# Kernel optimization log

Measured on AMD Instinct MI355X. Metric: run time of the kernel, lower is better.

## Reference

```python
import jax, jax.numpy as jnp
import numpy as np
from jax import lax

MASK_STEEP = 4.0
MASK_SHIFT = 0.5
RESIST_TH = 0.225
RESIST_STEEP = 50.0
MAX_DOSE = 1.02
MIN_DOSE = 0.98
KD = 35  # kernel_dim1 == kernel_dim2


def setup_inputs() -> dict:
    key = jax.random.key(0)
    ks = jax.random.split(key, 7)
    N, H, W, K = 2, 1024, 1024, 24
    return {
        "mask_tile": jax.random.uniform(ks[0], (N, 1, H, W), dtype=jnp.float32),
        "kernel_focus_r": jax.random.normal(ks[1], (K, KD, KD), dtype=jnp.float32) * 0.02,
        "kernel_focus_i": jax.random.normal(ks[2], (K, KD, KD), dtype=jnp.float32) * 0.02,
        "kernel_defocus_r": jax.random.normal(ks[3], (K, KD, KD), dtype=jnp.float32) * 0.02,
        "kernel_defocus_i": jax.random.normal(ks[4], (K, KD, KD), dtype=jnp.float32) * 0.02,
        "kernel_focus_scale": jax.random.uniform(ks[5], (K, 1, 1), dtype=jnp.float32),
        "kernel_defocus_scale": jax.random.uniform(ks[6], (K, 1, 1), dtype=jnp.float32),
    }


def _avepool3(x):
    # nn.AvgPool2d(kernel=3, stride=1, pad=1) with count_include_pad=True ==
    # conv with a 3x3 ones/9 kernel and zero padding.
    k = jnp.ones((1, 1, 3, 3), x.dtype) / 9.0
    return lax.conv_general_dilated(
        x, k, window_strides=(1, 1), padding=[(1, 1), (1, 1)],
        dimension_numbers=("NCHW", "OIHW", "NCHW"))


def _dose_branch(spec, dose, kernel, scale, h, w):
    # spec: [N,1,KD,KD] complex; kernel: [K,KD,KD] complex; scale: [K,1,1]
    x = (spec * dose) * kernel[None]                 # [N,K,KD,KD] (repeat_interleave via broadcast, C=1)
    x = jnp.fft.ifft2(x, s=(h, w))                   # zero-pad to full tile, [N,K,h,w] complex
    inten = (x.real * x.real + x.imag * x.imag) * scale[None]
    inten = jnp.sum(inten, axis=1, keepdims=True)    # [N,1,h,w]
    resist = jax.nn.sigmoid(RESIST_STEEP * (inten - RESIST_TH))
    return resist, inten


def reference(mask_tile, kernel_focus_r, kernel_focus_i, kernel_defocus_r,
              kernel_defocus_i, kernel_focus_scale, kernel_defocus_scale):
    n, _, h, w = mask_tile.shape
    off = h // 2 - KD // 2
    mask = _avepool3(mask_tile)
    mask = jax.nn.sigmoid(MASK_STEEP * (mask - MASK_SHIFT))
    mf = jnp.fft.fftshift(jnp.fft.fft2(mask), axes=(-2, -1))  # [N,1,h,w] complex64
    spec = mf[:, :, off:off + KD, off:off + KD]               # [N,1,KD,KD]
    kf = kernel_focus_r + 1j * kernel_focus_i
    kdf = kernel_defocus_r + 1j * kernel_defocus_i
    nominal, x_out = _dose_branch(spec, 1.0, kf, kernel_focus_scale, h, w)
    outer, x_out_max = _dose_branch(spec, MAX_DOSE, kf, kernel_focus_scale, h, w)
    inner, x_out_min = _dose_branch(spec, MIN_DOSE, kdf, kernel_defocus_scale, h, w)
    return (nominal, inner, outer, x_out, x_out_min, x_out_max)
```

## Files before the change

kernel.cpp:

```cpp
#include <hip/hip_runtime.h>
#include <math.h>

#define NBATCH 2
#define HH 1024
#define WW 1024
#define KKER 24
#define KDIM 35
#define NPIX (HH*WW)
#define KSQ (KDIM*KDIM)
#define NDA 69
#define NCH 7

#define TW_OFF   0
#define G_OFF    2048
#define SPEC_OFF (G_OFF + NBATCH*HH*KDIM*2)
#define VP_OFF   (SPEC_OFF + NBATCH*KSQ*2)
#define V_OFF    (VP_OFF + NBATCH*2*KKER*NCH*NDA*KDIM*2)
#define U_OFF    (V_OFF + NBATCH*2*NDA*KDIM*2)

__device__ __forceinline__ float2 cmadd(float2 p, float2 w, float2 u) {
    return make_float2(fmaf(p.x, w.x, fmaf(-p.y, w.y, u.x)),
                       fmaf(p.x, w.y, fmaf( p.y, w.x, u.y)));
}
__device__ __forceinline__ float sigm(float v) {
    return 1.f / (1.f + expf(-v));
}

__global__ void build_tw(float* __restrict__ ws) {
    int j = blockIdx.x * blockDim.x + threadIdx.x;
    if (j < 1024) {
        float s, c;
        sincospif(-2.0f * (float)j / 1024.0f, &s, &c);
        ws[TW_OFF + 2*j]     = c;
        ws[TW_OFF + 2*j + 1] = s;
    }
}

__global__ __launch_bounds__(512) void fwd_rows(const float* __restrict__ mt, float* __restrict__ ws) {
    __shared__ __align__(16) float vs[1024];
    __shared__ float row[1024];
    __shared__ float twl[2048];
    __shared__ float P[560 * 2];
    int bid = blockIdx.x;
    int n = bid >> 10, y = bid & 1023;
    int t = threadIdx.x;
    const float* base = mt + (size_t)n * NPIX;
    const float4* r0 = (y > 0)    ? (const float4*)(base + (size_t)(y - 1) * WW) : nullptr;
    const float4* r1 =              (const float4*)(base + (size_t)y * WW);
    const float4* r2 = (y < 1023) ? (const float4*)(base + (size_t)(y + 1) * WW) : nullptr;
    if (t < 256) {
        float4 a = r1[t];
        if (r0) { float4 b = r0[t]; a.x += b.x; a.y += b.y; a.z += b.z; a.w += b.w; }
        if (r2) { float4 b = r2[t]; a.x += b.x; a.y += b.y; a.z += b.z; a.w += b.w; }
        ((float4*)vs)[t] = a;
    }
    for (int i = t; i < 2048; i += 512) twl[i] = ws[TW_OFF + i];
    __syncthreads();
    for (int x = t; x < 1024; x += 512) {
        float s = vs[x];
        if (x > 0)    s += vs[x - 1];
        if (x < 1023) s += vs[x + 1];
        s *= (1.0f / 9.0f);
        row[x] = sigm(4.0f * (s - 0.5f));
    }
    __syncthreads();
    for (int task = t; task < 560; task += 512) {
        int q = task / KDIM, v = task - q * KDIM;
        int m = v - 17;
        unsigned jm = ((unsigned)m) & 1023u;
        float cmr = twl[2*jm], cmi = twl[2*jm + 1];
        float ar = 0.f, ai = 0.f;
        #pragma unroll
        for (int sc = 0; sc < 2; ++sc) {
            int xs = q * 64 + sc * 32;
            unsigned j0 = ((unsigned)(m * xs)) & 1023u;
            float wr = twl[2*j0], wi = twl[2*j0 + 1];
            #pragma unroll
            for (int i = 0; i < 32; ++i) {
                float val = row[xs + i];
                ar = fmaf(val, wr, ar);
                ai = fmaf(val, wi, ai);
                float nwr = fmaf(wr, cmr, -wi * cmi);
                float nwi = fmaf(wr, cmi,  wi * cmr);
                wr = nwr; wi = nwi;
            }
        }
        P[task * 2]     = ar;
        P[task * 2 + 1] = ai;
    }
    __syncthreads();
    if (t < KDIM) {
        float gr = 0.f, gi = 0.f;
        #pragma unroll
        for (int q = 0; q < 16; ++q) {
            gr += P[(q * KDIM + t) * 2];
            gi += P[(q * KDIM + t) * 2 + 1];
        }
        float* Gp = ws + G_OFF + ((size_t)(n * HH + y) * KDIM + t) * 2;
        Gp[0] = gr; Gp[1] = gi;
    }
}

__global__ __launch_bounds__(320) void fwd_cols(float* __restrict__ ws) {
    __shared__ float twl[2048];
    __shared__ float P[280 * 2];
    int bid = blockIdx.x;
    int n = bid / KDIM, a = bid - n * KDIM;
    int t = threadIdx.x;
    for (int i = t; i < 2048; i += 320) twl[i] = ws[TW_OFF + i];
    __syncthreads();
    int q = t / 40, b = t - 40 * q;
    if (b < KDIM) {
        int ma = a - 17;
        int y0 = q * 128;
        float ar = 0.f, ai = 0.f;
        for (int i = 0; i < 128; ++i) {
            int y = y0 + i;
            unsigned j = ((unsigned)(ma * y)) & 1023u;
            const float* Gp = ws + G_OFF + ((size_t)(n * HH + y) * KDIM + b) * 2;
            float gr = Gp[0], gi = Gp[1];
            float cr = twl[2*j], ci = twl[2*j + 1];
            ar = fmaf(gr, cr, ar); ar = fmaf(-gi, ci, ar);
            ai = fmaf(gr, ci, ai); ai = fmaf( gi, cr, ai);
        }
        P[(q * KDIM + b) * 2]     = ar;
        P[(q * KDIM + b) * 2 + 1] = ai;
    }
    __syncthreads();
    if (t < KDIM) {
        float sr = 0.f, si = 0.f;
        for (int qq = 0; qq < 8; ++qq) {
            sr += P[(qq * KDIM + t) * 2];
            si += P[(qq * KDIM + t) * 2 + 1];
        }
        float* Sp = ws + SPEC_OFF + ((size_t)(n * KDIM + a) * KDIM + t) * 2;
        Sp[0] = sr; Sp[1] = si;
    }
}

#define VROWS 103
#define VCOLS 43
__global__ __launch_bounds__(384) void mk_V(float* __restrict__ ws,
        const float* __restrict__ kfr, const float* __restrict__ kfi,
        const float* __restrict__ kdr, const float* __restrict__ kdi,
        const float* __restrict__ kfs, const float* __restrict__ kds) {
    __shared__ float2 Xp[VROWS * VCOLS];
    int bid = blockIdx.x;
    int c = bid % NCH; int r = bid / NCH;
    int k = r % KKER; r /= KKER;
    int br = r & 1; int n = r >> 1;
    int t = threadIdx.x;
    for (int i = t; i < VROWS * VCOLS; i += 384) Xp[i] = make_float2(0.f, 0.f);
    __syncthreads();
    const float* kr = (br ? kdr : kfr) + (size_t)k * KSQ;
    const float* ki = (br ? kdi : kfi) + (size_t)k * KSQ;
    const float* sp = ws + SPEC_OFF + (size_t)n * KSQ * 2;
    for (int i = t; i < KSQ; i += 384) {
        int a = i / KDIM, b = i - a * KDIM;
        float srr = sp[2*i], sii = sp[2*i + 1];
        float krr = kr[i], kii = ki[i];
        Xp[(a + 34) * VCOLS + b] = make_float2(srr * krr - sii * kii, srr * kii + sii * krr);
    }
    __syncthreads();
    const float INVN = 0x1p-40f;
    float s = (br ? kds[k] * (0.98f * 0.98f) : kfs[k]) * INVN;
    if (t < NDA * 5) {
        int dbg = t / NDA;
        int dai = t - dbg * NDA;
        int da  = dai - 34;
        int db0 = dbg * 8;
        int nbp = KDIM - db0;
        int ap0 = c * 5;
        int ap1 = ap0 + 5; if (ap1 > KDIM) ap1 = KDIM;
        float2 acc[8];
        #pragma unroll
        for (int j = 0; j < 8; ++j) acc[j] = make_float2(0.f, 0.f);
        for (int ap = ap0; ap < ap1; ++ap) {
            const float2* rx = Xp + (ap + da + 34) * VCOLS + db0;
            const float2* ry = Xp + (ap + 34) * VCOLS;
            float2 w[8];
            #pragma unroll
            for (int j = 0; j < 8; ++j) w[j] = rx[j];
            int bp = 0;
            for (; bp + 8 <= nbp; bp += 8) {
                #pragma unroll
                for (int u = 0; u < 8; ++u) {
                    float2 yv = ry[bp + u];
                    #pragma unroll
                    for (int j = 0; j < 8; ++j) {
                        acc[j].x = fmaf(w[j].x, yv.x, acc[j].x);
                        acc[j].x = fmaf(w[j].y, yv.y, acc[j].x);
                        acc[j].y = fmaf(w[j].y, yv.x, acc[j].y);
                        acc[j].y = fmaf(-w[j].x, yv.y, acc[j].y);
                    }
                    #pragma unroll
                    for (int j = 0; j < 7; ++j) w[j] = w[j + 1];
                    w[7] = rx[bp + u + 8];
                }
            }
            for (; bp < nbp; ++bp) {
                float2 yv = ry[bp];
                #pragma unroll
                for (int j = 0; j < 8; ++j) {
                    acc[j].x = fmaf(w[j].x, yv.x, acc[j].x);
                    acc[j].x = fmaf(w[j].y, yv.y, acc[j].x);
                    acc[j].y = fmaf(w[j].y, yv.x, acc[j].y);
                    acc[j].y = fmaf(-w[j].x, yv.y, acc[j].y);
                }
                #pragma unroll
                for (int j = 0; j < 7; ++j) w[j] = w[j + 1];
                w[7] = rx[bp + 8];
            }
        }
        int nb = n * 2 + br;
        size_t vb = ((((size_t)nb * KKER + k) * NCH + c) * NDA + dai) * KDIM;
        float* vp = ws + VP_OFF;
        #pragma unroll
        for (int j = 0; j < 8; ++j) {
            int db = db0 + j;
            if (db < KDIM) {
                vp[(vb + db) * 2]     = s * acc[j].x;
                vp[(vb + db) * 2 + 1] = s * acc[j].y;
            }
        }
    }
}

__global__ __launch_bounds__(320) void reduce_V(float* __restrict__ ws) {
    __shared__ float2 Ps[8][KDIM];
    int bid = blockIdx.x;
    int nb = bid / NDA, dai = bid - nb * NDA;
    int t = threadIdx.x;
    if (t < 8 * KDIM) {
        int g = t / KDIM, db = t - g * KDIM;
        const float* vp = ws + VP_OFF;
        float sr = 0.f, si = 0.f;
        #pragma unroll
        for (int j = 0; j < 21; ++j) {
            int kc = g + 8 * j;
            size_t idx = ((((size_t)nb * (KKER * NCH) + kc) * NDA + dai) * KDIM + db) * 2;
            sr += vp[idx]; si += vp[idx + 1];
        }
        Ps[g][db] = make_float2(sr, si);
    }
    __syncthreads();
    if (t < KDIM) {
        float sr = 0.f, si = 0.f;
        #pragma unroll
        for (int g = 0; g < 8; ++g) { sr += Ps[g][t].x; si += Ps[g][t].y; }
        size_t o = ((size_t)nb * NDA + dai) * KDIM + t;
        ws[V_OFF + o * 2]     = sr;
        ws[V_OFF + o * 2 + 1] = si;
    }
}

__global__ __launch_bounds__(256) void mk_U(float* __restrict__ ws) {
    __shared__ float2 Vl[NDA * KDIM];
    __shared__ float2 twl[1024];
    int bid = blockIdx.x;
    int yc = bid & 63; int nb = bid >> 6;
    int t = threadIdx.x;
    const float2* Vg = (const float2*)(ws + V_OFF) + (size_t)nb * NDA * KDIM;
    for (int i = t; i < NDA * KDIM; i += 256) Vl[i] = Vg[i];
    const float2* twg = (const float2*)(ws + TW_OFF);
    for (int i = t; i < 1024; i += 256) twl[i] = twg[i];
    __syncthreads();
    int n = nb >> 1, br = nb & 1;
    for (int task = t; task < 16 * KDIM; task += 256) {
        int yloc = task / KDIM, db = task - KDIM * yloc;
        int y = yc * 16 + yloc;
        float ar = 0.f, ai = 0.f;
        for (int dai = 0; dai < NDA; ++dai) {
            unsigned j = ((unsigned)(y * (dai - 34))) & 1023u;
            float2 cc = twl[j];
            float cr = cc.x, ci = -cc.y;
            float2 v = Vl[dai * KDIM + db];
            ar = fmaf(v.x, cr, ar); ar = fmaf(-v.y, ci, ar);
            ai = fmaf(v.x, ci, ai); ai = fmaf( v.y, cr, ai);
        }
        size_t ui = (((size_t)(n * HH + y) * 2 + br) * KDIM + db) * 2;
        ws[U_OFF + ui]     = ar;
        ws[U_OFF + ui + 1] = ai;
    }
}

__global__ __launch_bounds__(256) void litho_out(const float* __restrict__ ws,
                                                 float* __restrict__ out) {
    __shared__ float2 Ul[KDIM];
    int bid = blockIdx.x;
    int y = bid & 1023; int nb = bid >> 10;
    int n = nb >> 1, br = nb & 1;
    int t = threadIdx.x;
    const float2* Ug = (const float2*)(ws + U_OFF) + (((size_t)(n * HH + y)) * 2 + br) * KDIM;
    if (t < KDIM) Ul[t] = Ug[t];
    __syncthreads();
    const float2* twg = (const float2*)(ws + TW_OFF);
    float2 z  = twg[t];              z.y  = -z.y;
    float2 z2 = twg[(2*t) & 1023];   z2.y = -z2.y;
    float2 z3 = twg[(3*t) & 1023];   z3.y = -z3.y;
    float2 w  = twg[(4*t) & 1023];   w.y  = -w.y;
    float2 P0 = Ul[32], P1 = Ul[33], P2 = Ul[34], P3 = make_float2(0.f, 0.f);
    #pragma unroll
    for (int q = 7; q >= 0; --q) {
        float2 u0 = Ul[4*q], u1 = Ul[4*q+1], u2 = Ul[4*q+2], u3 = Ul[4*q+3];
        P0 = cmadd(P0, w, u0);
        P1 = cmadd(P1, w, u1);
        P2 = cmadd(P2, w, u2);
        P3 = cmadd(P3, w, u3);
    }
    float U0r = Ul[0].x;
    float A1x = P1.x * z.x  - P1.y * z.y,  A1y = P1.x * z.y  + P1.y * z.x;
    float A2x = P2.x * z2.x - P2.y * z2.y;
    float A3x = P3.x * z3.x - P3.y * z3.y, A3y = P3.x * z3.y + P3.y * z3.x;
    float Re4[4];
    Re4[0] = P0.x + A1x + A2x + A3x;
    Re4[1] = P0.x - A1y - A2x + A3y;
    Re4[2] = P0.x - A1x + A2x - A3x;
    Re4[3] = P0.x + A1y - A2x - A3y;
    size_t obase = (size_t)n * NPIX + (size_t)y * WW;
    const size_t OS = (size_t)NBATCH * NPIX;
    if (br == 0) {
        #pragma unroll
        for (int c = 0; c < 4; ++c) {
            int x = t + c * 256;
            float If   = fmaf(2.f, Re4[c], -U0r);
            float Imax = If * (1.02f * 1.02f);
            out[0 * OS + obase + x] = sigm(50.f * (If   - 0.225f));
            out[2 * OS + obase + x] = sigm(50.f * (Imax - 0.225f));
            out[3 * OS + obase + x] = If;
            out[5 * OS + obase + x] = Imax;
        }
    } else {
        #pragma unroll
        for (int c = 0; c < 4; ++c) {
            int x = t + c * 256;
            float Id = fmaf(2.f, Re4[c], -U0r);
            out[1 * OS + obase + x] = sigm(50.f * (Id - 0.225f));
            out[4 * OS + obase + x] = Id;
        }
    }
}

extern "C" void kernel_launch(void* const* d_in, const int* in_sizes, int n_in,
                              void* d_out, int out_size, void* d_ws, size_t ws_size,
                              hipStream_t stream) {
    (void)in_sizes; (void)n_in; (void)out_size; (void)ws_size;
    const float* mt  = (const float*)d_in[0];
    const float* kfr = (const float*)d_in[1];
    const float* kfi = (const float*)d_in[2];
    const float* kdr = (const float*)d_in[3];
    const float* kdi = (const float*)d_in[4];
    const float* kfs = (const float*)d_in[5];
    const float* kds = (const float*)d_in[6];
    float* out = (float*)d_out;
    float* ws  = (float*)d_ws;

    hipLaunchKernelGGL(build_tw,  dim3(4),                       dim3(256), 0, stream, ws);
    hipLaunchKernelGGL(fwd_rows,  dim3(NBATCH * HH),             dim3(512), 0, stream, mt, ws);
    hipLaunchKernelGGL(fwd_cols,  dim3(NBATCH * KDIM),           dim3(320), 0, stream, ws);
    hipLaunchKernelGGL(mk_V,      dim3(NBATCH * 2 * KKER * NCH), dim3(384), 0, stream,
                       ws, kfr, kfi, kdr, kdi, kfs, kds);
    hipLaunchKernelGGL(reduce_V,  dim3(NBATCH * 2 * NDA),        dim3(320), 0, stream, ws);
    hipLaunchKernelGGL(mk_U,      dim3(4 * 64),                  dim3(256), 0, stream, ws);
    hipLaunchKernelGGL(litho_out, dim3(NBATCH * 2 * HH),         dim3(256), 0, stream, ws, out);
}
```

Measured before the change: 166.3 us.

## Exploit Hermitian symmetry in forward DFT, fuse U build into output kernel

The forward row DFT now computes only the 18 non-negative frequencies of the real-valued mask row and fills the other half of the 35x35 spectrum by conjugate symmetry in fwd_cols, which roughly halves the forward DFT work and the G intermediate. Twiddle tables are built in shared memory inside each kernel with sincospif instead of a separate build_tw launch. The mk_U and litho_out kernels are merged, so each block computes the U rows for two output rows and writes the outputs directly, removing the U round-trip and two launches. In exchange, each block recomputes twiddles and reloads the V matrix, and a redundant dead store was added in reduce_V.

Measured after the change: 155.5 us. 6.5% less time.

```diff
diff --git a/kernel.cpp b/kernel.cpp
--- a/kernel.cpp
+++ b/kernel.cpp
@@ -10,13 +10,12 @@
 #define KSQ (KDIM*KDIM)
 #define NDA 69
 #define NCH 7
-
-#define TW_OFF   0
-#define G_OFF    2048
-#define SPEC_OFF (G_OFF + NBATCH*HH*KDIM*2)
+#define NFR 18
+
+#define G_OFF    0
+#define SPEC_OFF (G_OFF + NBATCH*HH*NFR*2)
 #define VP_OFF   (SPEC_OFF + NBATCH*KSQ*2)
 #define V_OFF    (VP_OFF + NBATCH*2*KKER*NCH*NDA*KDIM*2)
-#define U_OFF    (V_OFF + NBATCH*2*NDA*KDIM*2)
 
 __device__ __forceinline__ float2 cmadd(float2 p, float2 w, float2 u) {
     return make_float2(fmaf(p.x, w.x, fmaf(-p.y, w.y, u.x)),
@@ -26,115 +25,110 @@
     return 1.f / (1.f + expf(-v));
 }
 
-__global__ void build_tw(float* __restrict__ ws) {
-    int j = blockIdx.x * blockDim.x + threadIdx.x;
-    if (j < 1024) {
+__global__ __launch_bounds__(320) void fwd_rows(const float* __restrict__ mt, float* __restrict__ ws) {
+    __shared__ __align__(16) float vs[1024];
+    __shared__ float row[1056];
+    __shared__ float2 twl[1024];
+    __shared__ float2 P[16 * NFR];
+    int bid = blockIdx.x;
+    int n = bid >> 10, y = bid & 1023;
+    int t = threadIdx.x;
+    const float* base = mt + (size_t)n * NPIX;
+    if (t < 256) {
+        float4 a = ((const float4*)(base + (size_t)y * WW))[t];
+        if (y > 0)    { float4 b = ((const float4*)(base + (size_t)(y - 1) * WW))[t];
+                        a.x += b.x; a.y += b.y; a.z += b.z; a.w += b.w; }
+        if (y < 1023) { float4 b = ((const float4*)(base + (size_t)(y + 1) * WW))[t];
+                        a.x += b.x; a.y += b.y; a.z += b.z; a.w += b.w; }
+        ((float4*)vs)[t] = a;
+    }
+    for (int j = t; j < 1024; j += 320) {
         float s, c;
-        sincospif(-2.0f * (float)j / 1024.0f, &s, &c);
-        ws[TW_OFF + 2*j]     = c;
-        ws[TW_OFF + 2*j + 1] = s;
-    }
-}
-
-__global__ __launch_bounds__(512) void fwd_rows(const float* __restrict__ mt, float* __restrict__ ws) {
-    __shared__ __align__(16) float vs[1024];
-    __shared__ float row[1024];
-    __shared__ float twl[2048];
-    __shared__ float P[560 * 2];
-    int bid = blockIdx.x;
-    int n = bid >> 10, y = bid & 1023;
-    int t = threadIdx.x;
-    const float* base = mt + (size_t)n * NPIX;
-    const float4* r0 = (y > 0)    ? (const float4*)(base + (size_t)(y - 1) * WW) : nullptr;
-    const float4* r1 =              (const float4*)(base + (size_t)y * WW);
-    const float4* r2 = (y < 1023) ? (const float4*)(base + (size_t)(y + 1) * WW) : nullptr;
-    if (t < 256) {
-        float4 a = r1[t];
-        if (r0) { float4 b = r0[t]; a.x += b.x; a.y += b.y; a.z += b.z; a.w += b.w; }
-        if (r2) { float4 b = r2[t]; a.x += b.x; a.y += b.y; a.z += b.z; a.w += b.w; }
-        ((float4*)vs)[t] = a;
-    }
-    for (int i = t; i < 2048; i += 512) twl[i] = ws[TW_OFF + i];
-    __syncthreads();
-    for (int x = t; x < 1024; x += 512) {
+        sincospif(-2.0f * (float)j * (1.0f / 1024.0f), &s, &c);
+        twl[j] = make_float2(c, s);
+    }
+    __syncthreads();
+    for (int x = t; x < 1024; x += 320) {
         float s = vs[x];
         if (x > 0)    s += vs[x - 1];
         if (x < 1023) s += vs[x + 1];
         s *= (1.0f / 9.0f);
-        row[x] = sigm(4.0f * (s - 0.5f));
-    }
-    __syncthreads();
-    for (int task = t; task < 560; task += 512) {
-        int q = task / KDIM, v = task - q * KDIM;
-        int m = v - 17;
-        unsigned jm = ((unsigned)m) & 1023u;
-        float cmr = twl[2*jm], cmi = twl[2*jm + 1];
+        row[x + (x >> 5)] = sigm(4.0f * (s - 0.5f));
+    }
+    __syncthreads();
+    if (t < 16 * NFR) {
+        int q = t / NFR, m = t - q * NFR;
+        float2 cm = twl[m];
         float ar = 0.f, ai = 0.f;
         #pragma unroll
         for (int sc = 0; sc < 2; ++sc) {
             int xs = q * 64 + sc * 32;
             unsigned j0 = ((unsigned)(m * xs)) & 1023u;
-            float wr = twl[2*j0], wi = twl[2*j0 + 1];
+            float2 wv = twl[j0];
+            float wr = wv.x, wi = wv.y;
+            int rb = xs + (xs >> 5);
             #pragma unroll
             for (int i = 0; i < 32; ++i) {
-                float val = row[xs + i];
+                float val = row[rb + i];
                 ar = fmaf(val, wr, ar);
                 ai = fmaf(val, wi, ai);
-                float nwr = fmaf(wr, cmr, -wi * cmi);
-                float nwi = fmaf(wr, cmi,  wi * cmr);
+                float nwr = fmaf(wr, cm.x, -wi * cm.y);
+                float nwi = fmaf(wr, cm.y,  wi * cm.x);
                 wr = nwr; wi = nwi;
             }
         }
-        P[task * 2]     = ar;
-        P[task * 2 + 1] = ai;
-    }
-    __syncthreads();
-    if (t < KDIM) {
+        P[t] = make_float2(ar, ai);
+    }
+    __syncthreads();
+    if (t < NFR) {
         float gr = 0.f, gi = 0.f;
         #pragma unroll
         for (int q = 0; q < 16; ++q) {
-            gr += P[(q * KDIM + t) * 2];
-            gi += P[(q * KDIM + t) * 2 + 1];
-        }
-        float* Gp = ws + G_OFF + ((size_t)(n * HH + y) * KDIM + t) * 2;
-        Gp[0] = gr; Gp[1] = gi;
+            gr += P[q * NFR + t].x;
+            gi += P[q * NFR + t].y;
+        }
+        float2* Gp = (float2*)(ws + G_OFF) + (size_t)(n * HH + y) * NFR + t;
+        *Gp = make_float2(gr, gi);
     }
 }
 
 __global__ __launch_bounds__(320) void fwd_cols(float* __restrict__ ws) {
-    __shared__ float twl[2048];
-    __shared__ float P[280 * 2];
+    __shared__ float2 twl[1024];
+    __shared__ float2 P[16 * NFR];
     int bid = blockIdx.x;
     int n = bid / KDIM, a = bid - n * KDIM;
     int t = threadIdx.x;
-    for (int i = t; i < 2048; i += 320) twl[i] = ws[TW_OFF + i];
-    __syncthreads();
-    int q = t / 40, b = t - 40 * q;
-    if (b < KDIM) {
+    for (int j = t; j < 1024; j += 320) {
+        float s, c;
+        sincospif(-2.0f * (float)j * (1.0f / 1024.0f), &s, &c);
+        twl[j] = make_float2(c, s);
+    }
+    __syncthreads();
+    if (t < 16 * NFR) {
+        int g = t / NFR, mb = t - g * NFR;
         int ma = a - 17;
-        int y0 = q * 128;
+        int y0 = g * 64;
+        const float2* Gp = (const float2*)(ws + G_OFF) + (size_t)n * HH * NFR + mb;
         float ar = 0.f, ai = 0.f;
-        for (int i = 0; i < 128; ++i) {
+        for (int i = 0; i < 64; ++i) {
             int y = y0 + i;
             unsigned j = ((unsigned)(ma * y)) & 1023u;
-            const float* Gp = ws + G_OFF + ((size_t)(n * HH + y) * KDIM + b) * 2;
-            float gr = Gp[0], gi = Gp[1];
-            float cr = twl[2*j], ci = twl[2*j + 1];
-            ar = fmaf(gr, cr, ar); ar = fmaf(-gi, ci, ar);
-            ai = fmaf(gr, ci, ai); ai = fmaf( gi, cr, ai);
-        }
-        P[(q * KDIM + b) * 2]     = ar;
-        P[(q * KDIM + b) * 2 + 1] = ai;
-    }
-    __syncthreads();
-    if (t < KDIM) {
+            float2 g2 = Gp[(size_t)y * NFR];
+            float2 cc = twl[j];
+            ar = fmaf(g2.x, cc.x, ar); ar = fmaf(-g2.y, cc.y, ar);
+            ai = fmaf(g2.x, cc.y, ai); ai = fmaf( g2.y, cc.x, ai);
+        }
+        P[t] = make_float2(ar, ai);
+    }
+    __syncthreads();
+    if (t < NFR) {
         float sr = 0.f, si = 0.f;
-        for (int qq = 0; qq < 8; ++qq) {
-            sr += P[(qq * KDIM + t) * 2];
-            si += P[(qq * KDIM + t) * 2 + 1];
-        }
-        float* Sp = ws + SPEC_OFF + ((size_t)(n * KDIM + a) * KDIM + t) * 2;
-        Sp[0] = sr; Sp[1] = si;
+        #pragma unroll
+        for (int g = 0; g < 16; ++g) { sr += P[g * NFR + t].x; si += P[g * NFR + t].y; }
+        float2* Sp = (float2*)(ws + SPEC_OFF) + (size_t)n * KSQ;
+        Sp[a * KDIM + (17 + t)] = make_float2(sr, si);
+        if (t > 0)
+            Sp[(34 - a) * KDIM + (17 - t)] = make_float2(sr, -si);
     }
 }
 
@@ -250,25 +244,31 @@
         for (int g = 0; g < 8; ++g) { sr += Ps[g][t].x; si += Ps[g][t].y; }
         size_t o = ((size_t)nb * NDA + dai) * KDIM + t;
         ws[V_OFF + o * 2]     = sr;
+        ws[V_OFF + o * 2 + 1] = sr == sr ? si : si;
         ws[V_OFF + o * 2 + 1] = si;
     }
 }
 
-__global__ __launch_bounds__(256) void mk_U(float* __restrict__ ws) {
+#define YPB 2
+__global__ __launch_bounds__(256) void litho_fused(const float* __restrict__ ws,
+                                                   float* __restrict__ out) {
+    __shared__ float2 twl[1024];
     __shared__ float2 Vl[NDA * KDIM];
-    __shared__ float2 twl[1024];
-    int bid = blockIdx.x;
-    int yc = bid & 63; int nb = bid >> 6;
-    int t = threadIdx.x;
+    __shared__ float2 Ul[YPB][KDIM];
+    int bid = blockIdx.x;
+    int yc = bid & 511; int nb = bid >> 9;
+    int t = threadIdx.x;
+    for (int j = t; j < 1024; j += 256) {
+        float s, c;
+        sincospif(-2.0f * (float)j * (1.0f / 1024.0f), &s, &c);
+        twl[j] = make_float2(c, s);
+    }
     const float2* Vg = (const float2*)(ws + V_OFF) + (size_t)nb * NDA * KDIM;
     for (int i = t; i < NDA * KDIM; i += 256) Vl[i] = Vg[i];
-    const float2* twg = (const float2*)(ws + TW_OFF);
-    for (int i = t; i < 1024; i += 256) twl[i] = twg[i];
-    __syncthreads();
-    int n = nb >> 1, br = nb & 1;
-    for (int task = t; task < 16 * KDIM; task += 256) {
-        int yloc = task / KDIM, db = task - KDIM * yloc;
-        int y = yc * 16 + yloc;
+    __syncthreads();
+    if (t < YPB * KDIM) {
+        int yl = t / KDIM, db = t - yl * KDIM;
+        int y = yc * YPB + yl;
         float ar = 0.f, ai = 0.f;
         for (int dai = 0; dai < NDA; ++dai) {
             unsigned j = ((unsigned)(y * (dai - 34))) & 1023u;
@@ -278,65 +278,55 @@
             ar = fmaf(v.x, cr, ar); ar = fmaf(-v.y, ci, ar);
             ai = fmaf(v.x, ci, ai); ai = fmaf( v.y, cr, ai);
         }
-        size_t ui = (((size_t)(n * HH + y) * 2 + br) * KDIM + db) * 2;
-        ws[U_OFF + ui]     = ar;
-        ws[U_OFF + ui + 1] = ai;
-    }
-}
-
-__global__ __launch_bounds__(256) void litho_out(const float* __restrict__ ws,
-                                                 float* __restrict__ out) {
-    __shared__ float2 Ul[KDIM];
-    int bid = blockIdx.x;
-    int y = bid & 1023; int nb = bid >> 10;
+        Ul[yl][db] = make_float2(ar, ai);
+    }
+    __syncthreads();
     int n = nb >> 1, br = nb & 1;
-    int t = threadIdx.x;
-    const float2* Ug = (const float2*)(ws + U_OFF) + (((size_t)(n * HH + y)) * 2 + br) * KDIM;
-    if (t < KDIM) Ul[t] = Ug[t];
-    __syncthreads();
-    const float2* twg = (const float2*)(ws + TW_OFF);
-    float2 z  = twg[t];              z.y  = -z.y;
-    float2 z2 = twg[(2*t) & 1023];   z2.y = -z2.y;
-    float2 z3 = twg[(3*t) & 1023];   z3.y = -z3.y;
-    float2 w  = twg[(4*t) & 1023];   w.y  = -w.y;
-    float2 P0 = Ul[32], P1 = Ul[33], P2 = Ul[34], P3 = make_float2(0.f, 0.f);
+    float2 z  = twl[t];              z.y  = -z.y;
+    float2 z2 = twl[(2*t) & 1023];   z2.y = -z2.y;
+    float2 z3 = twl[(3*t) & 1023];   z3.y = -z3.y;
+    float2 w  = twl[(4*t) & 1023];   w.y  = -w.y;
+    const size_t OS = (size_t)NBATCH * NPIX;
     #pragma unroll
-    for (int q = 7; q >= 0; --q) {
-        float2 u0 = Ul[4*q], u1 = Ul[4*q+1], u2 = Ul[4*q+2], u3 = Ul[4*q+3];
-        P0 = cmadd(P0, w, u0);
-        P1 = cmadd(P1, w, u1);
-        P2 = cmadd(P2, w, u2);
-        P3 = cmadd(P3, w, u3);
-    }
-    float U0r = Ul[0].x;
-    float A1x = P1.x * z.x  - P1.y * z.y,  A1y = P1.x * z.y  + P1.y * z.x;
-    float A2x = P2.x * z2.x - P2.y * z2.y;
-    float A3x = P3.x * z3.x - P3.y * z3.y, A3y = P3.x * z3.y + P3.y * z3.x;
-    float Re4[4];
-    Re4[0] = P0.x + A1x + A2x + A3x;
-    Re4[1] = P0.x - A1y - A2x + A3y;
-    Re4[2] = P0.x - A1x + A2x - A3x;
-    Re4[3] = P0.x + A1y - A2x - A3y;
-    size_t obase = (size_t)n * NPIX + (size_t)y * WW;
-    const size_t OS = (size_t)NBATCH * NPIX;
-    if (br == 0) {
-        #pragma unroll
-        for (int c = 0; c < 4; ++c) {
-            int x = t + c * 256;
-            float If   = fmaf(2.f, Re4[c], -U0r);
-            float Imax = If * (1.02f * 1.02f);
-            out[0 * OS + obase + x] = sigm(50.f * (If   - 0.225f));
-            out[2 * OS + obase + x] = sigm(50.f * (Imax - 0.225f));
-            out[3 * OS + obase + x] = If;
-            out[5 * OS + obase + x] = Imax;
-        }
-    } else {
-        #pragma unroll
-        for (int c = 0; c < 4; ++c) {
-            int x = t + c * 256;
-            float Id = fmaf(2.f, Re4[c], -U0r);
-            out[1 * OS + obase + x] = sigm(50.f * (Id - 0.225f));
-            out[4 * OS + obase + x] = Id;
+    for (int yl = 0; yl < YPB; ++yl) {
+        int y = yc * YPB + yl;
+        float2 P0 = Ul[yl][32], P1 = Ul[yl][33], P2 = Ul[yl][34], P3 = make_float2(0.f, 0.f);
+        #pragma unroll
+        for (int q = 7; q >= 0; --q) {
+            P0 = cmadd(P0, w, Ul[yl][4*q]);
+            P1 = cmadd(P1, w, Ul[yl][4*q+1]);
+            P2 = cmadd(P2, w, Ul[yl][4*q+2]);
+            P3 = cmadd(P3, w, Ul[yl][4*q+3]);
+        }
+        float U0r = Ul[yl][0].x;
+        float A1x = P1.x * z.x  - P1.y * z.y,  A1y = P1.x * z.y  + P1.y * z.x;
+        float A2x = P2.x * z2.x - P2.y * z2.y;
+        float A3x = P3.x * z3.x - P3.y * z3.y, A3y = P3.x * z3.y + P3.y * z3.x;
+        float Re4[4];
+        Re4[0] = P0.x + A1x + A2x + A3x;
+        Re4[1] = P0.x - A1y - A2x + A3y;
+        Re4[2] = P0.x - A1x + A2x - A3x;
+        Re4[3] = P0.x + A1y - A2x - A3y;
+        size_t obase = (size_t)n * NPIX + (size_t)y * WW;
+        if (br == 0) {
+            #pragma unroll
+            for (int c = 0; c < 4; ++c) {
+                int x = t + c * 256;
+                float If   = fmaf(2.f, Re4[c], -U0r);
+                float Imax = If * (1.02f * 1.02f);
+                out[0 * OS + obase + x] = sigm(50.f * (If   - 0.225f));
+                out[2 * OS + obase + x] = sigm(50.f * (Imax - 0.225f));
+                out[3 * OS + obase + x] = If;
+                out[5 * OS + obase + x] = Imax;
+            }
+        } else {
+            #pragma unroll
+            for (int c = 0; c < 4; ++c) {
+                int x = t + c * 256;
+                float Id = fmaf(2.f, Re4[c], -U0r);
+                out[1 * OS + obase + x] = sigm(50.f * (Id - 0.225f));
+                out[4 * OS + obase + x] = Id;
+            }
         }
     }
 }
@@ -355,12 +345,10 @@
     float* out = (float*)d_out;
     float* ws  = (float*)d_ws;
 
-    hipLaunchKernelGGL(build_tw,  dim3(4),                       dim3(256), 0, stream, ws);
-    hipLaunchKernelGGL(fwd_rows,  dim3(NBATCH * HH),             dim3(512), 0, stream, mt, ws);
-    hipLaunchKernelGGL(fwd_cols,  dim3(NBATCH * KDIM),           dim3(320), 0, stream, ws);
-    hipLaunchKernelGGL(mk_V,      dim3(NBATCH * 2 * KKER * NCH), dim3(384), 0, stream,
+    hipLaunchKernelGGL(fwd_rows,    dim3(NBATCH * HH),             dim3(320), 0, stream, mt, ws);
+    hipLaunchKernelGGL(fwd_cols,    dim3(NBATCH * KDIM),           dim3(320), 0, stream, ws);
+    hipLaunchKernelGGL(mk_V,        dim3(NBATCH * 2 * KKER * NCH), dim3(384), 0, stream,
                        ws, kfr, kfi, kdr, kdi, kfs, kds);
-    hipLaunchKernelGGL(reduce_V,  dim3(NBATCH * 2 * NDA),        dim3(320), 0, stream, ws);
-    hipLaunchKernelGGL(mk_U,      dim3(4 * 64),                  dim3(256), 0, stream, ws);
-    hipLaunchKernelGGL(litho_out, dim3(NBATCH * 2 * HH),         dim3(256), 0, stream, ws, out);
-}
+    hipLaunchKernelGGL(reduce_V,    dim3(NBATCH * 2 * NDA),        dim3(320), 0, stream, ws);
+    hipLaunchKernelGGL(litho_fused, dim3(NBATCH * 2 * 512),        dim3(256), 0, stream, ws, out);
+}
```
